# Kernel tuning notes

Hardware: AMD Instinct MI355X
Metric: run time of the kernel (lower is better)

## Reference

```python
import jax, jax.numpy as jnp
import numpy as np

B, D, T, NT, DS, G = 1024, 512, 36, 64, 32, 4
EPS = 1e-5


def setup_inputs() -> dict:
    key = jax.random.key(0)
    ks = jax.random.split(key, 8)
    return {
        "x": jax.random.normal(ks[0], (B, D, T, 1), jnp.float32),
        "y": jax.random.normal(ks[1], (B, D, T, 1), jnp.float32),
        "my_tokens": jax.random.normal(ks[2], (NT, D), jnp.float32) * 0.02,
        "gate": jax.random.normal(ks[3], (1,), jnp.float32) * 0.1,
        "gate_av": jax.random.normal(ks[4], (1,), jnp.float32) * 0.1,
        "w_down": jax.random.normal(ks[5], (DS, D // G), jnp.float32) * 0.05,  # Conv2d(512->32,1,groups=4) weight [32,128,1,1] squeezed
        "w_up": jax.random.normal(ks[6], (D, DS // G), jnp.float32) * 0.05,    # Conv2d(32->512,1,groups=4) weight [512,8,1,1] squeezed
        "bn1_g": jnp.ones((DS,), jnp.float32), "bn1_b": jnp.zeros((DS,), jnp.float32),
        "bn2_g": jnp.ones((D,), jnp.float32), "bn2_b": jnp.zeros((D,), jnp.float32),
        "lnb_g": jnp.ones((D,), jnp.float32), "lnb_b": jnp.zeros((D,), jnp.float32),
        "lnp_g": jnp.ones((D,), jnp.float32), "lnp_b": jnp.zeros((D,), jnp.float32),
    }


def _layernorm(h, g, b):  # normalize last dim
    mu = jnp.mean(h, axis=-1, keepdims=True)
    var = jnp.var(h, axis=-1, keepdims=True)
    return (h - mu) * jax.lax.rsqrt(var + EPS) * g + b


def _batchnorm(z, g, b):  # z: [B,C,T], training-mode batch stats over (B,T)
    mu = jnp.mean(z, axis=(0, 2), keepdims=True)
    var = jnp.var(z, axis=(0, 2), keepdims=True)
    return (z - mu) * jax.lax.rsqrt(var + EPS) * g[None, :, None] + b[None, :, None]


def reference(x, y, my_tokens, gate, gate_av, w_down, w_up,
              bn1_g, bn1_b, bn2_g, bn2_b, lnb_g, lnb_b, lnp_g, lnp_b):
    xs = x[..., 0]  # [B,D,T]
    ys = y[..., 0]  # [B,D,T]
    # token <- y cross attention
    att_y2tk = jax.nn.softmax(jnp.einsum('td,bds->bts', my_tokens, ys), axis=-1)  # [B,NT,T]
    rep = my_tokens[None] + jnp.einsum('bts,bds->btd', att_y2tk, ys)  # [B,NT,D]
    # x <- token cross attention
    att_tk2x = jax.nn.softmax(jnp.einsum('bds,btd->bst', xs, rep), axis=-1)  # [B,T,NT]
    x_res = jnp.einsum('bst,btd->bsd', att_tk2x, rep)  # [B,T,D]
    xc = xs + gate_av[0] * jnp.swapaxes(x_res, 1, 2)  # [B,D,T]
    # ln_before over channel dim
    h = jnp.swapaxes(_layernorm(jnp.swapaxes(xc, 1, 2), lnb_g, lnb_b), 1, 2)  # [B,D,T]
    # grouped 1x1 down conv
    hg = h.reshape(h.shape[0], G, D // G, T)
    z = jnp.einsum('bgct,goc->bgot', hg, w_down.reshape(G, DS // G, D // G)).reshape(h.shape[0], DS, T)
    z = jax.nn.relu(_batchnorm(z, bn1_g, bn1_b))
    # grouped 1x1 up conv
    zg = z.reshape(z.shape[0], G, DS // G, T)
    o = jnp.einsum('bgct,goc->bgot', zg, w_up.reshape(G, D // G, DS // G)).reshape(z.shape[0], D, T)
    o = _batchnorm(o, bn2_g, bn2_b)
    o = jnp.swapaxes(_layernorm(jnp.swapaxes(o, 1, 2), lnp_g, lnp_b), 1, 2)
    return (gate[0] * o)[..., None]  # [B,D,T,1]
```

## Files before the change

### kernel.cpp

```cpp
#include <hip/hip_runtime.h>

#define B_ 1024
#define D_ 512
#define T_ 36
#define NT_ 64
#define DS_ 32
#define EPS_ 1e-5f

typedef float f32x4 __attribute__((ext_vector_type(4)));
typedef __bf16 bf16x8 __attribute__((ext_vector_type(8)));
typedef unsigned short u16x8 __attribute__((ext_vector_type(8)));

#define DEVI static __device__ __forceinline__
#define MFMA16 __builtin_amdgcn_mfma_f32_16x16x32_bf16

DEVI unsigned short f2bf(float f) { return __builtin_bit_cast(unsigned short, (__bf16)f); }
DEVI float bf2f(unsigned short h) { return (float)__builtin_bit_cast(__bf16, h); }

DEVI unsigned swz(int row, int col) {
    return (unsigned)(row * 1024 + ((2 * col) ^ ((row & 7) << 4)));
}

#define OFF_YST 0
#define OFF_XST 49152
#define OFF_SC  98304
#define OFF_A1  109056
#define OFF_A1T 118272
#define OFF_A2  125184
#define OFF_GT  132096
#define OFF_W   139008
#define K1_LDS  145920

__global__ __launch_bounds__(512)
void k0_prepack(const float* __restrict__ tok, const float* __restrict__ wd,
                unsigned short* __restrict__ tokbf, unsigned short* __restrict__ tokT,
                unsigned short* __restrict__ wdd)
{
    int i = blockIdx.x * 512 + threadIdx.x;
    if (i < 32768) {
        tokbf[i] = f2bf(tok[i]);
    } else if (i < 65536) {
        int j = i - 32768; int d = j >> 6, t = j & 63;
        tokT[j] = f2bf(tok[t * 512 + d]);
    } else if (i < 81920) {
        int j = i - 65536; int o = j >> 9, dd = j & 511;
        wdd[j] = ((dd >> 7) == (o >> 3)) ? f2bf(wd[o * 128 + (dd & 127)]) : (unsigned short)0;
    }
}

__global__ __launch_bounds__(1024, 4)
void k1_fused(const float* __restrict__ x, const float* __restrict__ y,
              const unsigned short* __restrict__ tokbf, const unsigned short* __restrict__ tokT,
              const float* __restrict__ gav_p, const unsigned short* __restrict__ wdd,
              const float* __restrict__ lnbg, const float* __restrict__ lnbb,
              float* __restrict__ z_pre)
{
    extern __shared__ char lds[];
    float* sc = (float*)(lds + OFF_SC);
    unsigned short* a1  = (unsigned short*)(lds + OFF_A1);
    unsigned short* a1t = (unsigned short*)(lds + OFF_A1T);
    unsigned short* a2  = (unsigned short*)(lds + OFF_A2);
    unsigned short* gt  = (unsigned short*)(lds + OFF_GT);
    unsigned short* wb  = (unsigned short*)(lds + OFF_W);

    const int b    = blockIdx.x;
    const int tid  = threadIdx.x;
    const int lane = tid & 63;
    const int w    = tid >> 6;
    const int l15  = lane & 15;
    const int l4   = lane >> 4;

    const float* yb = y + b * (D_ * T_);
    const float* xb = x + b * (D_ * T_);

    {
        unsigned* z1 = (unsigned*)(lds + OFF_YST + 36 * 1024);
        unsigned* z2 = (unsigned*)(lds + OFF_XST + 36 * 1024);
        for (int i = tid; i < 3072; i += 1024) { z1[i] = 0u; z2[i] = 0u; }
        unsigned* z3 = (unsigned*)(lds + OFF_A1);
        for (int i = tid; i < 9216; i += 1024) z3[i] = 0u;
    }
    for (int ww = tid; ww < 1152; ww += 1024) {
        int isx = (ww >= 576) ? 1 : 0;
        int u = isx ? (ww - 576) : ww;
        const float* src = isx ? xb : yb;
        char* dst = lds + (isx ? OFF_XST : OFF_YST);
        int dblk = u / 9, s4 = u - dblk * 9;
        int s0 = s4 * 4;
        const float* bp = src + dblk * 8 * T_ + s0;
        u16x8 u0, u1, u2, u3;
        #pragma unroll
        for (int r = 0; r < 8; ++r) {
            f32x4 v = *(const f32x4*)(bp + r * T_);
            u0[r] = f2bf(v[0]); u1[r] = f2bf(v[1]);
            u2[r] = f2bf(v[2]); u3[r] = f2bf(v[3]);
        }
        *(u16x8*)(dst + swz(s0 + 0, dblk * 8)) = u0;
        *(u16x8*)(dst + swz(s0 + 1, dblk * 8)) = u1;
        *(u16x8*)(dst + swz(s0 + 2, dblk * 8)) = u2;
        *(u16x8*)(dst + swz(s0 + 3, dblk * 8)) = u3;
    }
    __syncthreads();

    for (int tile = w; tile < 21; tile += 16) {
        f32x4 acc = {0.f, 0.f, 0.f, 0.f};
        if (tile < 12) {
            int mt = tile / 3, nt = tile % 3;
            int trow = mt * 16 + l15, srow = nt * 16 + l15;
            for (int ks = 0; ks < 16; ++ks) {
                int k0 = ks * 32 + l4 * 8;
                bf16x8 af = *(const bf16x8*)(tokbf + trow * 512 + k0);
                bf16x8 bv = *(const bf16x8*)(lds + OFF_YST + swz(srow, k0));
                acc = MFMA16(af, bv, acc, 0, 0, 0);
            }
            if (srow < T_) {
                #pragma unroll
                for (int j = 0; j < 4; ++j)
                    sc[(mt * 16 + l4 * 4 + j) * 42 + srow] = acc[j];
            }
        } else {
            int g = tile - 12;
            int mt = g / 3, nt = g % 3;
            int arow = mt * 16 + l15, brow = nt * 16 + l15;
            for (int ks = 0; ks < 16; ++ks) {
                int k0 = ks * 32 + l4 * 8;
                bf16x8 af = *(const bf16x8*)(lds + OFF_XST + swz(arow, k0));
                bf16x8 bv = *(const bf16x8*)(lds + OFF_YST + swz(brow, k0));
                acc = MFMA16(af, bv, acc, 0, 0, 0);
            }
            #pragma unroll
            for (int j = 0; j < 4; ++j)
                gt[(mt * 16 + l4 * 4 + j) * 72 + brow] = f2bf(acc[j]);
        }
    }
    __syncthreads();

    {
        int t = tid >> 4, l16 = tid & 15;
        const float* scp = sc + t * 42;
        float v0 = scp[l16];
        float v1 = scp[l16 + 16];
        float v2 = (l16 < 4) ? scp[l16 + 32] : -1e30f;
        float m = fmaxf(fmaxf(v0, v1), v2);
        #pragma unroll
        for (int off = 1; off < 16; off <<= 1) m = fmaxf(m, __shfl_xor(m, off));
        float e0 = __expf(v0 - m), e1 = __expf(v1 - m);
        float e2 = (l16 < 4) ? __expf(v2 - m) : 0.f;
        float ssum = e0 + e1 + e2;
        #pragma unroll
        for (int off = 1; off < 16; off <<= 1) ssum += __shfl_xor(ssum, off);
        float inv = 1.f / ssum;
        unsigned short h0 = f2bf(e0 * inv), h1 = f2bf(e1 * inv);
        a1[t * 72 + l16] = h0;       a1[t * 72 + l16 + 16] = h1;
        a1t[l16 * 72 + t] = h0;      a1t[(l16 + 16) * 72 + t] = h1;
        if (l16 < 4) {
            unsigned short h2 = f2bf(e2 * inv);
            a1[t * 72 + l16 + 32] = h2;
            a1t[(l16 + 32) * 72 + t] = h2;
        }
    }
    __syncthreads();

    if (w < 12) {
        int mt = w / 3, nt = w % 3;
        int trow = mt * 16 + l15, srow = nt * 16 + l15;
        f32x4 acc = {0.f, 0.f, 0.f, 0.f};
        for (int ks = 0; ks < 16; ++ks) {
            int k0 = ks * 32 + l4 * 8;
            bf16x8 af = *(const bf16x8*)(tokbf + trow * 512 + k0);
            bf16x8 bv = *(const bf16x8*)(lds + OFF_XST + swz(srow, k0));
            acc = MFMA16(af, bv, acc, 0, 0, 0);
        }
        #pragma unroll
        for (int ks = 0; ks < 2; ++ks) {
            int k0 = ks * 32 + l4 * 8;
            bf16x8 af = *(const bf16x8*)(a1 + trow * 72 + k0);
            bf16x8 bv = *(const bf16x8*)(gt + srow * 72 + k0);
            acc = MFMA16(af, bv, acc, 0, 0, 0);
        }
        if (srow < T_) {
            #pragma unroll
            for (int j = 0; j < 4; ++j)
                sc[(mt * 16 + l4 * 4 + j) * 42 + srow] = acc[j];
        }
    }
    __syncthreads();

    if (tid < 768) {
        int s = tid >> 4, l16 = tid & 15;
        if (s < T_) {
            float v0 = sc[(l16) * 42 + s];
            float v1 = sc[(l16 + 16) * 42 + s];
            float v2 = sc[(l16 + 32) * 42 + s];
            float v3 = sc[(l16 + 48) * 42 + s];
            float m = fmaxf(fmaxf(v0, v1), fmaxf(v2, v3));
            #pragma unroll
            for (int off = 1; off < 16; off <<= 1) m = fmaxf(m, __shfl_xor(m, off));
            float e0 = __expf(v0 - m), e1 = __expf(v1 - m), e2 = __expf(v2 - m), e3 = __expf(v3 - m);
            float ssum = e0 + e1 + e2 + e3;
            #pragma unroll
            for (int off = 1; off < 16; off <<= 1) ssum += __shfl_xor(ssum, off);
            float inv = 1.f / ssum;
            a2[s * 72 + l16]      = f2bf(e0 * inv);
            a2[s * 72 + l16 + 16] = f2bf(e1 * inv);
            a2[s * 72 + l16 + 32] = f2bf(e2 * inv);
            a2[s * 72 + l16 + 48] = f2bf(e3 * inv);
        }
    }
    __syncthreads();

    if (w < 9) {
        int mt = w / 3, nt = w % 3;
        f32x4 acc = {0.f, 0.f, 0.f, 0.f};
        #pragma unroll
        for (int ks = 0; ks < 2; ++ks) {
            int k0 = ks * 32 + l4 * 8;
            bf16x8 af = *(const bf16x8*)(a2 + (mt * 16 + l15) * 72 + k0);
            bf16x8 bv = *(const bf16x8*)(a1t + (nt * 16 + l15) * 72 + k0);
            acc = MFMA16(af, bv, acc, 0, 0, 0);
        }
        #pragma unroll
        for (int j = 0; j < 4; ++j)
            wb[(mt * 16 + l4 * 4 + j) * 72 + nt * 16 + l15] = f2bf(acc[j]);
    }
    __syncthreads();

    {
        const float gav = gav_p[0];
        f32x4 acc[2][3];
        #pragma unroll
        for (int mi = 0; mi < 2; ++mi)
            #pragma unroll
            for (int n = 0; n < 3; ++n) acc[mi][n] = (f32x4){0.f, 0.f, 0.f, 0.f};

        bf16x8 aT[2][2], aY[2][2];
        #pragma unroll
        for (int mi = 0; mi < 2; ++mi) {
            int d = (2 * w + mi) * 16 + l15;
            aT[mi][0] = *(const bf16x8*)(tokT + d * 64 + l4 * 8);
            aT[mi][1] = *(const bf16x8*)(tokT + d * 64 + 32 + l4 * 8);
            const float* yrow = yb + d * T_;
            f32x4 p0 = *(const f32x4*)(yrow + l4 * 8);
            f32x4 p1 = *(const f32x4*)(yrow + l4 * 8 + 4);
            bf16x8 t0, t1;
            #pragma unroll
            for (int j = 0; j < 4; ++j) { t0[j] = (__bf16)p0[j]; t0[4 + j] = (__bf16)p1[j]; }
            if (l4 == 0) {
                f32x4 p2 = *(const f32x4*)(yrow + 32);
                #pragma unroll
                for (int j = 0; j < 4; ++j) { t1[j] = (__bf16)p2[j]; t1[4 + j] = (__bf16)0.f; }
            } else {
                #pragma unroll
                for (int j = 0; j < 8; ++j) t1[j] = (__bf16)0.f;
            }
            aY[mi][0] = t0; aY[mi][1] = t1;
        }
        #pragma unroll
        for (int n = 0; n < 3; ++n) {
            int srow = n * 16 + l15;
            bf16x8 b20 = *(const bf16x8*)(a2 + srow * 72 + l4 * 8);
            bf16x8 b21 = *(const bf16x8*)(a2 + srow * 72 + 32 + l4 * 8);
            bf16x8 bw0 = *(const bf16x8*)(wb + srow * 72 + l4 * 8);
            bf16x8 bw1 = *(const bf16x8*)(wb + srow * 72 + 32 + l4 * 8);
            #pragma unroll
            for (int mi = 0; mi < 2; ++mi) {
                acc[mi][n] = MFMA16(aT[mi][0], b20, acc[mi][n], 0, 0, 0);
                acc[mi][n] = MFMA16(aT[mi][1], b21, acc[mi][n], 0, 0, 0);
                acc[mi][n] = MFMA16(aY[mi][0], bw0, acc[mi][n], 0, 0, 0);
                acc[mi][n] = MFMA16(aY[mi][1], bw1, acc[mi][n], 0, 0, 0);
            }
        }

        float* red = sc;
        float rs_[3] = {0.f, 0.f, 0.f}, rq_[3] = {0.f, 0.f, 0.f};
        #pragma unroll
        for (int mi = 0; mi < 2; ++mi) {
            #pragma unroll
            for (int n = 0; n < 3; ++n) {
                int s = n * 16 + l15;
                if (s < T_) {
                    #pragma unroll
                    for (int j = 0; j < 4; ++j) {
                        int d = (2 * w + mi) * 16 + l4 * 4 + j;
                        float xsv = bf2f(*(const unsigned short*)(lds + OFF_XST + swz(s, d)));
                        float v = xsv + gav * acc[mi][n][j];
                        acc[mi][n][j] = v;
                        rs_[n] += v; rq_[n] += v * v;
                    }
                }
            }
        }
        #pragma unroll
        for (int n = 0; n < 3; ++n) {
            rs_[n] += __shfl_xor(rs_[n], 16); rq_[n] += __shfl_xor(rq_[n], 16);
            rs_[n] += __shfl_xor(rs_[n], 32); rq_[n] += __shfl_xor(rq_[n], 32);
        }
        if (l4 == 0) {
            #pragma unroll
            for (int n = 0; n < 3; ++n) {
                int s = n * 16 + l15;
                if (s < T_) { red[s * 16 + w] = rs_[n]; red[768 + s * 16 + w] = rq_[n]; }
            }
        }
        __syncthreads();
        if (tid < T_) {
            int s = tid; float S = 0.f, Q = 0.f;
            #pragma unroll
            for (int q = 0; q < 16; ++q) { S += red[s * 16 + q]; Q += red[768 + s * 16 + q]; }
            float mu = S * (1.f / 512.f);
            float var = Q * (1.f / 512.f) - mu * mu;
            red[1536 + s] = mu; red[1584 + s] = rsqrtf(var + EPS_);
        }
        __syncthreads();

        float lg[2][4], lbv[2][4];
        #pragma unroll
        for (int mi = 0; mi < 2; ++mi)
            #pragma unroll
            for (int j = 0; j < 4; ++j) {
                int d = (2 * w + mi) * 16 + l4 * 4 + j;
                lg[mi][j] = lnbg[d]; lbv[mi][j] = lnbb[d];
            }
        #pragma unroll
        for (int mi = 0; mi < 2; ++mi) {
            #pragma unroll
            for (int n = 0; n < 3; ++n) {
                int s = n * 16 + l15;
                if (s < T_) {
                    float mu = red[1536 + s], rsg = red[1584 + s];
                    #pragma unroll
                    for (int j = 0; j < 4; ++j) {
                        int d = (2 * w + mi) * 16 + l4 * 4 + j;
                        *(unsigned short*)(lds + OFF_YST + swz(s, d)) =
                            f2bf((acc[mi][n][j] - mu) * rsg * lg[mi][j] + lbv[mi][j]);
                    }
                }
            }
        }
    }
    __syncthreads();

    if (w < 6) {
        int mt = w / 3, nt = w % 3;
        int orow = mt * 16 + l15, srow = nt * 16 + l15;
        f32x4 acc = {0.f, 0.f, 0.f, 0.f};
        for (int ks = 0; ks < 16; ++ks) {
            int k0 = ks * 32 + l4 * 8;
            bf16x8 af = *(const bf16x8*)(wdd + orow * 512 + k0);
            bf16x8 bv = *(const bf16x8*)(lds + OFF_YST + swz(srow, k0));
            acc = MFMA16(af, bv, acc, 0, 0, 0);
        }
        if (srow < T_) {
            #pragma unroll
            for (int j = 0; j < 4; ++j)
                z_pre[b * (DS_ * T_) + (mt * 16 + l4 * 4 + j) * T_ + srow] = acc[j];
        }
    }
}

__global__ __launch_bounds__(256)
void k3a_bn1part(const float* __restrict__ z_pre, float* __restrict__ p3)
{
    __shared__ float rbuf[4][2];
    int blk = blockIdx.x;
    int o = blk & 31, sl = blk >> 5;
    int tid = threadIdx.x;
    float S = 0.f, Q = 0.f;
    for (int i = tid; i < 64 * T_; i += 256) {
        int bb = sl * 64 + i / T_, t = i - (i / T_) * T_;
        float v = z_pre[bb * (DS_ * T_) + o * T_ + t];
        S += v; Q += v * v;
    }
    #pragma unroll
    for (int off = 1; off < 64; off <<= 1) { S += __shfl_xor(S, off); Q += __shfl_xor(Q, off); }
    int ww = tid >> 6;
    if ((tid & 63) == 0) { rbuf[ww][0] = S; rbuf[ww][1] = Q; }
    __syncthreads();
    if (tid == 0) {
        float s2 = 0.f, q2 = 0.f;
        for (int i = 0; i < 4; ++i) { s2 += rbuf[i][0]; q2 += rbuf[i][1]; }
        p3[blk * 2] = s2; p3[blk * 2 + 1] = q2;
    }
}

__global__ __launch_bounds__(64)
void k3b_bn1stats(const float* __restrict__ p3, float* __restrict__ st1)
{
    int o = threadIdx.x;
    if (o < 32) {
        float S = 0.f, Q = 0.f;
        for (int sl = 0; sl < 16; ++sl) {
            S += p3[((sl << 5) | o) * 2];
            Q += p3[((sl << 5) | o) * 2 + 1];
        }
        float mu = S / 36864.f;
        float var = Q / 36864.f - mu * mu;
        st1[o] = mu; st1[32 + o] = rsqrtf(var + EPS_);
    }
}

__global__ __launch_bounds__(256)
void k4m_moments(const float* __restrict__ z_pre, const float* __restrict__ st1,
                 const float* __restrict__ g1p, const float* __restrict__ b1p,
                 float* __restrict__ m4)
{
    __shared__ float zr[32][40];
    int blk = blockIdx.x, tid = threadIdx.x;
    int c2 = tid & 7, c1 = (tid >> 3) & 7, g = tid >> 6;
    int ch1 = g * 8 + c1, ch2 = g * 8 + c2;
    float acc = 0.f, asum = 0.f;
    for (int bi = 0; bi < 16; ++bi) {
        int b = blk * 16 + bi;
        __syncthreads();
        for (int i = tid; i < DS_ * T_; i += 256) {
            int o = i / T_, t = i - o * T_;
            float v = z_pre[b * (DS_ * T_) + i];
            zr[o][t] = fmaxf(0.f, (v - st1[o]) * st1[32 + o] * g1p[o] + b1p[o]);
        }
        __syncthreads();
        for (int t = 0; t < T_; ++t) {
            float a = zr[ch1][t], b2 = zr[ch2][t];
            acc += a * b2;
            asum += a;
        }
    }
    m4[blk * 288 + tid] = acc;
    if (c1 == c2) m4[blk * 288 + 256 + g * 8 + c1] = asum;
}

__global__ __launch_bounds__(512)
void k4s_bn2stats(const float* __restrict__ m4, const float* __restrict__ wu,
                  float* __restrict__ st2)
{
    __shared__ float M2[256], mz[32];
    int tid = threadIdx.x;
    if (tid < 256) {
        float S = 0.f;
        for (int k = 0; k < 64; ++k) S += m4[k * 288 + tid];
        M2[tid] = S * (1.f / 36864.f);
    } else if (tid < 288) {
        int j = tid - 256;
        float S = 0.f;
        for (int k = 0; k < 64; ++k) S += m4[k * 288 + 256 + j];
        mz[j] = S * (1.f / 36864.f);
    }
    __syncthreads();
    int d = tid, g = d >> 7;
    float wr[8];
    #pragma unroll
    for (int c = 0; c < 8; ++c) wr[c] = wu[d * 8 + c];
    float mu2 = 0.f;
    #pragma unroll
    for (int c = 0; c < 8; ++c) mu2 += wr[c] * mz[g * 8 + c];
    float e2 = 0.f;
    #pragma unroll
    for (int c = 0; c < 8; ++c)
        #pragma unroll
        for (int c2 = 0; c2 < 8; ++c2)
            e2 += wr[c] * wr[c2] * M2[g * 64 + c * 8 + c2];
    st2[d] = mu2;
    st2[512 + d] = rsqrtf(e2 - mu2 * mu2 + EPS_);
}

#define K5_LDS 47888
__global__ __launch_bounds__(512, 6)
void k5_final(const float* __restrict__ z_pre, const float* __restrict__ st1,
              const float* __restrict__ g1p, const float* __restrict__ b1p,
              const float* __restrict__ wu, const float* __restrict__ st2,
              const float* __restrict__ g2p, const float* __restrict__ b2p,
              const float* __restrict__ lnpg, const float* __restrict__ lnpb,
              const float* __restrict__ gate_p, float* __restrict__ out)
{
    extern __shared__ char lds[];
    unsigned short* o_f = (unsigned short*)lds;
    float* zrT = (float*)(lds + 41984);
    int b = blockIdx.x;
    int tid = threadIdx.x;

    for (int i = tid; i < DS_ * T_; i += 512) {
        int o = i / T_, s = i - o * T_;
        float v = z_pre[b * (DS_ * T_) + i];
        zrT[s * 41 + o] = fmaxf(0.f, (v - st1[o]) * st1[32 + o] * g1p[o] + b1p[o]);
    }
    __syncthreads();

    for (int i = tid; i < D_ * T_; i += 512) {
        int d = i / T_, t = i - d * T_;
        const float* zp = &zrT[t * 41 + (d >> 7) * 8];
        const float* wp = &wu[d * 8];
        f32x4 w0 = *(const f32x4*)wp;
        f32x4 w1 = *(const f32x4*)(wp + 4);
        float acc = zp[0]*w0[0] + zp[1]*w0[1] + zp[2]*w0[2] + zp[3]*w0[3]
                  + zp[4]*w1[0] + zp[5]*w1[1] + zp[6]*w1[2] + zp[7]*w1[3];
        o_f[d * 41 + t] = f2bf((acc - st2[d]) * st2[512 + d] * g2p[d] + b2p[d]);
    }
    __syncthreads();

    int w = tid >> 6, lane = tid & 63;
    float gate = gate_p[0];
    for (int t = w; t < T_; t += 8) {
        float S = 0.f, Q = 0.f;
        float v[8];
        #pragma unroll
        for (int i2 = 0; i2 < 8; ++i2) {
            float vv = bf2f(o_f[(i2 * 64 + lane) * 41 + t]);
            v[i2] = vv; S += vv; Q += vv * vv;
        }
        #pragma unroll
        for (int off = 1; off < 64; off <<= 1) { S += __shfl_xor(S, off); Q += __shfl_xor(Q, off); }
        float mu = S * (1.f / 512.f);
        float var = Q * (1.f / 512.f) - mu * mu;
        float rs = rsqrtf(var + EPS_);
        #pragma unroll
        for (int i2 = 0; i2 < 8; ++i2) {
            int d = i2 * 64 + lane;
            o_f[d * 41 + t] = f2bf(gate * ((v[i2] - mu) * rs * lnpg[d] + lnpb[d]));
        }
    }
    __syncthreads();

    float* ob = out + b * (D_ * T_);
    for (int i = tid; i < D_ * T_; i += 512) {
        int d = i / T_, t = i - d * T_;
        ob[i] = bf2f(o_f[d * 41 + t]);
    }
}

extern "C" void kernel_launch(void* const* d_in, const int* in_sizes, int n_in,
                              void* d_out, int out_size, void* d_ws, size_t ws_size,
                              hipStream_t stream)
{
    (void)in_sizes; (void)n_in; (void)out_size; (void)ws_size;
    const float* x    = (const float*)d_in[0];
    const float* y    = (const float*)d_in[1];
    const float* tok  = (const float*)d_in[2];
    const float* gate = (const float*)d_in[3];
    const float* gav  = (const float*)d_in[4];
    const float* wd   = (const float*)d_in[5];
    const float* wu   = (const float*)d_in[6];
    const float* bn1g = (const float*)d_in[7];
    const float* bn1b = (const float*)d_in[8];
    const float* bn2g = (const float*)d_in[9];
    const float* bn2b = (const float*)d_in[10];
    const float* lnbg = (const float*)d_in[11];
    const float* lnbb = (const float*)d_in[12];
    const float* lnpg = (const float*)d_in[13];
    const float* lnpb = (const float*)d_in[14];
    float* out = (float*)d_out;

    char* ws = (char*)d_ws;
    float* z_pre          = (float*)ws;
    float* st1            = (float*)(ws + 4718592);
    unsigned short* tokbf = (unsigned short*)(ws + 4719104);
    unsigned short* tokT  = (unsigned short*)(ws + 4784640);
    unsigned short* wdd   = (unsigned short*)(ws + 4850176);
    float* p3             = (float*)(ws + 4882944);
    float* m4             = (float*)(ws + 4887040);
    float* st2            = (float*)(ws + 4960768);

    hipFuncSetAttribute((const void*)k1_fused, hipFuncAttributeMaxDynamicSharedMemorySize, K1_LDS);
    hipFuncSetAttribute((const void*)k5_final, hipFuncAttributeMaxDynamicSharedMemorySize, K5_LDS);

    k0_prepack<<<160, 512, 0, stream>>>(tok, wd, tokbf, tokT, wdd);
    k1_fused<<<B_, 1024, K1_LDS, stream>>>(x, y, tokbf, tokT, gav, wdd, lnbg, lnbb, z_pre);
    k3a_bn1part<<<512, 256, 0, stream>>>(z_pre, p3);
    k3b_bn1stats<<<1, 64, 0, stream>>>(p3, st1);
    k4m_moments<<<64, 256, 0, stream>>>(z_pre, st1, bn1g, bn1b, m4);
    k4s_bn2stats<<<1, 512, 0, stream>>>(m4, wu, st2);
    k5_final<<<B_, 512, K5_LDS, stream>>>(z_pre, st1, bn1g, bn1b, wu, st2, bn2g, bn2b,
                                          lnpg, lnpb, gate, out);
}
```

Measured before the change: 201.3 us.

## Overlap x staging with first GEMM, split MFMA chains, merge BN1 stat kernels

In the fused kernel, y is staged first and x is staged by idle waves while other waves compute the token-y scores. The 36x36 x·y^T tile count is trimmed to 9 and the 16-step MFMA loops use two independent accumulators to shorten dependency chains. The y prefetch for a later stage is moved earlier, and scalar LDS and global loads are vectorised. The two-kernel BN1 statistics reduction is merged into one 32-block kernel and the moments kernel gets twice the blocks. The single-pass BN1 reduction over 32 blocks may have poor parallelism, which could offset the saved launch.

```diff
diff --git a/kernel.cpp b/kernel.cpp
--- a/kernel.cpp
+++ b/kernel.cpp
@@ -10,6 +10,7 @@
 typedef float f32x4 __attribute__((ext_vector_type(4)));
 typedef __bf16 bf16x8 __attribute__((ext_vector_type(8)));
 typedef unsigned short u16x8 __attribute__((ext_vector_type(8)));
+typedef unsigned short u16x4 __attribute__((ext_vector_type(4)));
 
 #define DEVI static __device__ __forceinline__
 #define MFMA16 __builtin_amdgcn_mfma_f32_16x16x32_bf16
@@ -21,7 +22,30 @@
     return (unsigned)(row * 1024 + ((2 * col) ^ ((row & 7) << 4)));
 }
 
-#define OFF_YST 0
+DEVI f32x4 tile16_gl(const unsigned short* __restrict__ Arow, const char* img, int brow, int l4)
+{
+    f32x4 acc0 = {0.f,0.f,0.f,0.f}, acc1 = {0.f,0.f,0.f,0.f};
+    #pragma unroll
+    for (int ks = 0; ks < 16; ks += 2) {
+        int ka = ks * 32 + l4 * 8, kb = ka + 32;
+        acc0 = MFMA16(*(const bf16x8*)(Arow + ka), *(const bf16x8*)(img + swz(brow, ka)), acc0, 0, 0, 0);
+        acc1 = MFMA16(*(const bf16x8*)(Arow + kb), *(const bf16x8*)(img + swz(brow, kb)), acc1, 0, 0, 0);
+    }
+    return acc0 + acc1;
+}
+
+DEVI f32x4 tile16_ll(const char* imgA, int arow, const char* imgB, int brow, int l4)
+{
+    f32x4 acc0 = {0.f,0.f,0.f,0.f}, acc1 = {0.f,0.f,0.f,0.f};
+    #pragma unroll
+    for (int ks = 0; ks < 16; ks += 2) {
+        int ka = ks * 32 + l4 * 8, kb = ka + 32;
+        acc0 = MFMA16(*(const bf16x8*)(imgA + swz(arow, ka)), *(const bf16x8*)(imgB + swz(brow, ka)), acc0, 0, 0, 0);
+        acc1 = MFMA16(*(const bf16x8*)(imgA + swz(arow, kb)), *(const bf16x8*)(imgB + swz(brow, kb)), acc1, 0, 0, 0);
+    }
+    return acc0 + acc1;
+}
+
 #define OFF_XST 49152
 #define OFF_SC  98304
 #define OFF_A1  109056
@@ -48,6 +72,24 @@
     }
 }
 
+DEVI void stage_unit(const float* __restrict__ src, char* __restrict__ dst, int u)
+{
+    int dblk = u / 9, s4 = u - dblk * 9;
+    int s0 = s4 * 4;
+    const float* bp = src + dblk * 8 * T_ + s0;
+    u16x8 u0, u1, u2, u3;
+    #pragma unroll
+    for (int r = 0; r < 8; ++r) {
+        f32x4 v = *(const f32x4*)(bp + r * T_);
+        u0[r] = f2bf(v[0]); u1[r] = f2bf(v[1]);
+        u2[r] = f2bf(v[2]); u3[r] = f2bf(v[3]);
+    }
+    *(u16x8*)(dst + swz(s0 + 0, dblk * 8)) = u0;
+    *(u16x8*)(dst + swz(s0 + 1, dblk * 8)) = u1;
+    *(u16x8*)(dst + swz(s0 + 2, dblk * 8)) = u2;
+    *(u16x8*)(dst + swz(s0 + 3, dblk * 8)) = u3;
+}
+
 __global__ __launch_bounds__(1024, 4)
 void k1_fused(const float* __restrict__ x, const float* __restrict__ y,
               const unsigned short* __restrict__ tokbf, const unsigned short* __restrict__ tokT,
@@ -73,64 +115,42 @@
     const float* yb = y + b * (D_ * T_);
     const float* xb = x + b * (D_ * T_);
 
-    {
-        unsigned* z1 = (unsigned*)(lds + OFF_YST + 36 * 1024);
+    if (tid < 576) {
+        stage_unit(yb, lds, tid);
+    } else {
+        int z = tid - 576;
+        unsigned* z1 = (unsigned*)(lds + 36 * 1024);
+        for (int i = z; i < 3072; i += 448) z1[i] = 0u;
         unsigned* z2 = (unsigned*)(lds + OFF_XST + 36 * 1024);
-        for (int i = tid; i < 3072; i += 1024) { z1[i] = 0u; z2[i] = 0u; }
+        for (int i = z; i < 3072; i += 448) z2[i] = 0u;
         unsigned* z3 = (unsigned*)(lds + OFF_A1);
-        for (int i = tid; i < 9216; i += 1024) z3[i] = 0u;
-    }
-    for (int ww = tid; ww < 1152; ww += 1024) {
-        int isx = (ww >= 576) ? 1 : 0;
-        int u = isx ? (ww - 576) : ww;
-        const float* src = isx ? xb : yb;
-        char* dst = lds + (isx ? OFF_XST : OFF_YST);
-        int dblk = u / 9, s4 = u - dblk * 9;
-        int s0 = s4 * 4;
-        const float* bp = src + dblk * 8 * T_ + s0;
-        u16x8 u0, u1, u2, u3;
-        #pragma unroll
-        for (int r = 0; r < 8; ++r) {
-            f32x4 v = *(const f32x4*)(bp + r * T_);
-            u0[r] = f2bf(v[0]); u1[r] = f2bf(v[1]);
-            u2[r] = f2bf(v[2]); u3[r] = f2bf(v[3]);
-        }
-        *(u16x8*)(dst + swz(s0 + 0, dblk * 8)) = u0;
-        *(u16x8*)(dst + swz(s0 + 1, dblk * 8)) = u1;
-        *(u16x8*)(dst + swz(s0 + 2, dblk * 8)) = u2;
-        *(u16x8*)(dst + swz(s0 + 3, dblk * 8)) = u3;
-    }
-    __syncthreads();
-
-    for (int tile = w; tile < 21; tile += 16) {
-        f32x4 acc = {0.f, 0.f, 0.f, 0.f};
-        if (tile < 12) {
-            int mt = tile / 3, nt = tile % 3;
-            int trow = mt * 16 + l15, srow = nt * 16 + l15;
-            for (int ks = 0; ks < 16; ++ks) {
-                int k0 = ks * 32 + l4 * 8;
-                bf16x8 af = *(const bf16x8*)(tokbf + trow * 512 + k0);
-                bf16x8 bv = *(const bf16x8*)(lds + OFF_YST + swz(srow, k0));
-                acc = MFMA16(af, bv, acc, 0, 0, 0);
-            }
-            if (srow < T_) {
-                #pragma unroll
-                for (int j = 0; j < 4; ++j)
-                    sc[(mt * 16 + l4 * 4 + j) * 42 + srow] = acc[j];
-            }
-        } else {
-            int g = tile - 12;
-            int mt = g / 3, nt = g % 3;
-            int arow = mt * 16 + l15, brow = nt * 16 + l15;
-            for (int ks = 0; ks < 16; ++ks) {
-                int k0 = ks * 32 + l4 * 8;
-                bf16x8 af = *(const bf16x8*)(lds + OFF_XST + swz(arow, k0));
-                bf16x8 bv = *(const bf16x8*)(lds + OFF_YST + swz(brow, k0));
-                acc = MFMA16(af, bv, acc, 0, 0, 0);
-            }
+        for (int i = z; i < 9216; i += 448) z3[i] = 0u;
+    }
+    __syncthreads();
+
+    if (w < 12) {
+        int mt = w / 3, nt = w % 3;
+        int trow = mt * 16 + l15, srow = nt * 16 + l15;
+        f32x4 acc = tile16_gl(tokbf + trow * 512, lds, srow, l4);
+        if (srow < T_) {
             #pragma unroll
             for (int j = 0; j < 4; ++j)
-                gt[(mt * 16 + l4 * 4 + j) * 72 + brow] = f2bf(acc[j]);
+                sc[(mt * 16 + l4 * 4 + j) * 42 + srow] = acc[j];
+        }
+    } else {
+        for (int u = tid - 768; u < 576; u += 256)
+            stage_unit(xb, lds + OFF_XST, u);
+    }
+    __syncthreads();
+
+    if (w < 9) {
+        int mt = w / 3, nt = w % 3;
+        int arow = mt * 16 + l15, brow = nt * 16 + l15;
+        f32x4 acc = tile16_ll(lds + OFF_XST, arow, lds, brow, l4);
+        #pragma unroll
+        for (int j = 0; j < 4; ++j) {
+            int gr = mt * 16 + l4 * 4 + j;
+            if (gr < T_) gt[gr * 72 + brow] = f2bf(acc[j]);
         }
     }
     __syncthreads();
@@ -159,25 +179,27 @@
             a1t[(l16 + 32) * 72 + t] = h2;
         }
     }
+    f32x4 py0[2], py1[2], py2[2];
+    #pragma unroll
+    for (int mi = 0; mi < 2; ++mi) {
+        const float* yrow = yb + ((2 * w + mi) * 16 + l15) * T_;
+        py0[mi] = *(const f32x4*)(yrow + l4 * 8);
+        py1[mi] = *(const f32x4*)(yrow + l4 * 8 + 4);
+        if (l4 == 0) py2[mi] = *(const f32x4*)(yrow + 32);
+        else         py2[mi] = (f32x4){0.f, 0.f, 0.f, 0.f};
+    }
     __syncthreads();
 
     if (w < 12) {
         int mt = w / 3, nt = w % 3;
         int trow = mt * 16 + l15, srow = nt * 16 + l15;
-        f32x4 acc = {0.f, 0.f, 0.f, 0.f};
-        for (int ks = 0; ks < 16; ++ks) {
-            int k0 = ks * 32 + l4 * 8;
-            bf16x8 af = *(const bf16x8*)(tokbf + trow * 512 + k0);
-            bf16x8 bv = *(const bf16x8*)(lds + OFF_XST + swz(srow, k0));
-            acc = MFMA16(af, bv, acc, 0, 0, 0);
-        }
-        #pragma unroll
-        for (int ks = 0; ks < 2; ++ks) {
-            int k0 = ks * 32 + l4 * 8;
-            bf16x8 af = *(const bf16x8*)(a1 + trow * 72 + k0);
-            bf16x8 bv = *(const bf16x8*)(gt + srow * 72 + k0);
-            acc = MFMA16(af, bv, acc, 0, 0, 0);
-        }
+        bf16x8 sa0 = *(const bf16x8*)(a1 + trow * 72 + l4 * 8);
+        bf16x8 sa1 = *(const bf16x8*)(a1 + trow * 72 + 32 + l4 * 8);
+        bf16x8 sb0 = *(const bf16x8*)(gt + srow * 72 + l4 * 8);
+        bf16x8 sb1 = *(const bf16x8*)(gt + srow * 72 + 32 + l4 * 8);
+        f32x4 acc = tile16_gl(tokbf + trow * 512, lds + OFF_XST, srow, l4);
+        acc = MFMA16(sa0, sb0, acc, 0, 0, 0);
+        acc = MFMA16(sa1, sb1, acc, 0, 0, 0);
         if (srow < T_) {
             #pragma unroll
             for (int j = 0; j < 4; ++j)
@@ -215,9 +237,8 @@
         #pragma unroll
         for (int ks = 0; ks < 2; ++ks) {
             int k0 = ks * 32 + l4 * 8;
-            bf16x8 af = *(const bf16x8*)(a2 + (mt * 16 + l15) * 72 + k0);
-            bf16x8 bv = *(const bf16x8*)(a1t + (nt * 16 + l15) * 72 + k0);
-            acc = MFMA16(af, bv, acc, 0, 0, 0);
+            acc = MFMA16(*(const bf16x8*)(a2 + (mt * 16 + l15) * 72 + k0),
+                         *(const bf16x8*)(a1t + (nt * 16 + l15) * 72 + k0), acc, 0, 0, 0);
         }
         #pragma unroll
         for (int j = 0; j < 4; ++j)
@@ -239,19 +260,11 @@
             int d = (2 * w + mi) * 16 + l15;
             aT[mi][0] = *(const bf16x8*)(tokT + d * 64 + l4 * 8);
             aT[mi][1] = *(const bf16x8*)(tokT + d * 64 + 32 + l4 * 8);
-            const float* yrow = yb + d * T_;
-            f32x4 p0 = *(const f32x4*)(yrow + l4 * 8);
-            f32x4 p1 = *(const f32x4*)(yrow + l4 * 8 + 4);
             bf16x8 t0, t1;
             #pragma unroll
-            for (int j = 0; j < 4; ++j) { t0[j] = (__bf16)p0[j]; t0[4 + j] = (__bf16)p1[j]; }
-            if (l4 == 0) {
-                f32x4 p2 = *(const f32x4*)(yrow + 32);
-                #pragma unroll
-                for (int j = 0; j < 4; ++j) { t1[j] = (__bf16)p2[j]; t1[4 + j] = (__bf16)0.f; }
-            } else {
-                #pragma unroll
-                for (int j = 0; j < 8; ++j) t1[j] = (__bf16)0.f;
+            for (int j = 0; j < 4; ++j) {
+                t0[j] = (__bf16)py0[mi][j]; t0[4 + j] = (__bf16)py1[mi][j];
+                t1[j] = (__bf16)py2[mi][j]; t1[4 + j] = (__bf16)0.f;
             }
             aY[mi][0] = t0; aY[mi][1] = t1;
         }
@@ -275,15 +288,15 @@
         float rs_[3] = {0.f, 0.f, 0.f}, rq_[3] = {0.f, 0.f, 0.f};
         #pragma unroll
         for (int mi = 0; mi < 2; ++mi) {
+            int dcol = (2 * w + mi) * 16 + l4 * 4;
             #pragma unroll
             for (int n = 0; n < 3; ++n) {
                 int s = n * 16 + l15;
                 if (s < T_) {
+                    u16x4 xv = *(const u16x4*)(lds + OFF_XST + swz(s, dcol));
                     #pragma unroll
                     for (int j = 0; j < 4; ++j) {
-                        int d = (2 * w + mi) * 16 + l4 * 4 + j;
-                        float xsv = bf2f(*(const unsigned short*)(lds + OFF_XST + swz(s, d)));
-                        float v = xsv + gav * acc[mi][n][j];
+                        float v = bf2f(xv[j]) + gav * acc[mi][n][j];
                         acc[mi][n][j] = v;
                         rs_[n] += v; rq_[n] += v * v;
                     }
@@ -313,27 +326,21 @@
         }
         __syncthreads();
 
-        float lg[2][4], lbv[2][4];
-        #pragma unroll
-        for (int mi = 0; mi < 2; ++mi)
-            #pragma unroll
-            for (int j = 0; j < 4; ++j) {
-                int d = (2 * w + mi) * 16 + l4 * 4 + j;
-                lg[mi][j] = lnbg[d]; lbv[mi][j] = lnbb[d];
-            }
         #pragma unroll
         for (int mi = 0; mi < 2; ++mi) {
+            int dcol = (2 * w + mi) * 16 + l4 * 4;
+            f32x4 gv  = *(const f32x4*)(lnbg + dcol);
+            f32x4 bv2 = *(const f32x4*)(lnbb + dcol);
             #pragma unroll
             for (int n = 0; n < 3; ++n) {
                 int s = n * 16 + l15;
                 if (s < T_) {
                     float mu = red[1536 + s], rsg = red[1584 + s];
+                    u16x4 hv;
                     #pragma unroll
-                    for (int j = 0; j < 4; ++j) {
-                        int d = (2 * w + mi) * 16 + l4 * 4 + j;
-                        *(unsigned short*)(lds + OFF_YST + swz(s, d)) =
-                            f2bf((acc[mi][n][j] - mu) * rsg * lg[mi][j] + lbv[mi][j]);
-                    }
+                    for (int j = 0; j < 4; ++j)
+                        hv[j] = f2bf((acc[mi][n][j] - mu) * rsg * gv[j] + bv2[j]);
+                    *(u16x4*)(lds + swz(s, dcol)) = hv;
                 }
             }
         }
@@ -343,13 +350,7 @@
     if (w < 6) {
         int mt = w / 3, nt = w % 3;
         int orow = mt * 16 + l15, srow = nt * 16 + l15;
-        f32x4 acc = {0.f, 0.f, 0.f, 0.f};
-        for (int ks = 0; ks < 16; ++ks) {
-            int k0 = ks * 32 + l4 * 8;
-            bf16x8 af = *(const bf16x8*)(wdd + orow * 512 + k0);
-            bf16x8 bv = *(const bf16x8*)(lds + OFF_YST + swz(srow, k0));
-            acc = MFMA16(af, bv, acc, 0, 0, 0);
-        }
+        f32x4 acc = tile16_gl(wdd + orow * 512, lds, srow, l4);
         if (srow < T_) {
             #pragma unroll
             for (int j = 0; j < 4; ++j)
@@ -359,16 +360,15 @@
 }
 
 __global__ __launch_bounds__(256)
-void k3a_bn1part(const float* __restrict__ z_pre, float* __restrict__ p3)
+void k3_bn1(const float* __restrict__ z_pre, float* __restrict__ st1)
 {
     __shared__ float rbuf[4][2];
-    int blk = blockIdx.x;
-    int o = blk & 31, sl = blk >> 5;
+    int o = blockIdx.x;
     int tid = threadIdx.x;
     float S = 0.f, Q = 0.f;
-    for (int i = tid; i < 64 * T_; i += 256) {
-        int bb = sl * 64 + i / T_, t = i - (i / T_) * T_;
-        float v = z_pre[bb * (DS_ * T_) + o * T_ + t];
+    for (int i = tid; i < B_ * T_; i += 256) {
+        int b = i / T_, t = i - b * T_;
+        float v = z_pre[b * (DS_ * T_) + o * T_ + t];
         S += v; Q += v * v;
     }
     #pragma unroll
@@ -379,22 +379,8 @@
     if (tid == 0) {
         float s2 = 0.f, q2 = 0.f;
         for (int i = 0; i < 4; ++i) { s2 += rbuf[i][0]; q2 += rbuf[i][1]; }
-        p3[blk * 2] = s2; p3[blk * 2 + 1] = q2;
-    }
-}
-
-__global__ __launch_bounds__(64)
-void k3b_bn1stats(const float* __restrict__ p3, float* __restrict__ st1)
-{
-    int o = threadIdx.x;
-    if (o < 32) {
-        float S = 0.f, Q = 0.f;
-        for (int sl = 0; sl < 16; ++sl) {
-            S += p3[((sl << 5) | o) * 2];
-            Q += p3[((sl << 5) | o) * 2 + 1];
-        }
-        float mu = S / 36864.f;
-        float var = Q / 36864.f - mu * mu;
+        float mu = s2 / 36864.f;
+        float var = q2 / 36864.f - mu * mu;
         st1[o] = mu; st1[32 + o] = rsqrtf(var + EPS_);
     }
 }
@@ -409,8 +395,8 @@
     int c2 = tid & 7, c1 = (tid >> 3) & 7, g = tid >> 6;
     int ch1 = g * 8 + c1, ch2 = g * 8 + c2;
     float acc = 0.f, asum = 0.f;
-    for (int bi = 0; bi < 16; ++bi) {
-        int b = blk * 16 + bi;
+    for (int bi = 0; bi < 8; ++bi) {
+        int b = blk * 8 + bi;
         __syncthreads();
         for (int i = tid; i < DS_ * T_; i += 256) {
             int o = i / T_, t = i - o * T_;
@@ -436,12 +422,12 @@
     int tid = threadIdx.x;
     if (tid < 256) {
         float S = 0.f;
-        for (int k = 0; k < 64; ++k) S += m4[k * 288 + tid];
+        for (int k = 0; k < 128; ++k) S += m4[k * 288 + tid];
         M2[tid] = S * (1.f / 36864.f);
     } else if (tid < 288) {
         int j = tid - 256;
         float S = 0.f;
-        for (int k = 0; k < 64; ++k) S += m4[k * 288 + 256 + j];
+        for (int k = 0; k < 128; ++k) S += m4[k * 288 + 256 + j];
         mz[j] = S * (1.f / 36864.f);
     }
     __syncthreads();
@@ -554,18 +540,16 @@
     unsigned short* tokbf = (unsigned short*)(ws + 4719104);
     unsigned short* tokT  = (unsigned short*)(ws + 4784640);
     unsigned short* wdd   = (unsigned short*)(ws + 4850176);
-    float* p3             = (float*)(ws + 4882944);
-    float* m4             = (float*)(ws + 4887040);
-    float* st2            = (float*)(ws + 4960768);
+    float* m4             = (float*)(ws + 4882944);
+    float* st2            = (float*)(ws + 5030400);
 
     hipFuncSetAttribute((const void*)k1_fused, hipFuncAttributeMaxDynamicSharedMemorySize, K1_LDS);
     hipFuncSetAttribute((const void*)k5_final, hipFuncAttributeMaxDynamicSharedMemorySize, K5_LDS);
 
     k0_prepack<<<160, 512, 0, stream>>>(tok, wd, tokbf, tokT, wdd);
     k1_fused<<<B_, 1024, K1_LDS, stream>>>(x, y, tokbf, tokT, gav, wdd, lnbg, lnbb, z_pre);
-    k3a_bn1part<<<512, 256, 0, stream>>>(z_pre, p3);
-    k3b_bn1stats<<<1, 64, 0, stream>>>(p3, st1);
-    k4m_moments<<<64, 256, 0, stream>>>(z_pre, st1, bn1g, bn1b, m4);
+    k3_bn1<<<DS_, 256, 0, stream>>>(z_pre, st1);
+    k4m_moments<<<128, 256, 0, stream>>>(z_pre, st1, bn1g, bn1b, m4);
     k4s_bn2stats<<<1, 512, 0, stream>>>(m4, wu, st2);
     k5_final<<<B_, 512, K5_LDS, stream>>>(z_pre, st1, bn1g, bn1b, wu, st2, bn2g, bn2b,
                                           lnpg, lnpb, gate, out);
```

Result: slower. 224.7 us (+11.6%).
